# Performance work log

Measured on AMD Instinct MI355X. Metric: run time of the kernel, lower is better.

The kernel has to match this reference:

```python
import jax, jax.numpy as jnp
import numpy as np

NZ, NC = 100, 2
FEAT_NUMBER, FEATURE_DIM = 8192, 1024
B = 8192
BN_EPS = 1e-5
GUMBEL_EPS = 0.001
TEMP = 0.1


def _batchnorm(h, gamma, beta):
    # torch BatchNorm1d training mode: biased batch statistics
    mu = jnp.mean(h, axis=0, keepdims=True)
    var = jnp.var(h, axis=0, keepdims=True)
    return (h - mu) * jax.lax.rsqrt(var + BN_EPS) * gamma + beta


def setup_inputs() -> dict:
    key = jax.random.key(0)
    ks = jax.random.split(key, 16)
    def glorot(k, shape):
        lim = 1.0 / np.sqrt(shape[0])
        return jax.random.uniform(k, shape, jnp.float32, -lim, lim)
    return {
        "x": jax.random.normal(ks[0], (B, NZ), jnp.float32),
        "y": jax.random.uniform(ks[1], (B, NC), jnp.float32),
        "W1": glorot(ks[2], (NZ + NC, 256)), "b1": jnp.zeros((256,), jnp.float32),
        "g1": jnp.ones((256,), jnp.float32), "be1": jnp.zeros((256,), jnp.float32),
        "W2": glorot(ks[3], (256, 64)), "b2": jnp.zeros((64,), jnp.float32),
        "g2": jnp.ones((64,), jnp.float32), "be2": jnp.zeros((64,), jnp.float32),
        "W3": glorot(ks[4], (64, FEAT_NUMBER)), "b3": jnp.zeros((FEAT_NUMBER,), jnp.float32),
        "codebook": jax.random.normal(ks[5], (FEAT_NUMBER, FEATURE_DIM), jnp.float32),
    }


def reference(x, y, W1, b1, g1, be1, W2, b2, g2, be2, W3, b3, codebook):
    z = jnp.concatenate([x, y], axis=-1)                       # [B, nz+nc]
    h = jax.nn.relu(_batchnorm(z @ W1 + b1, g1, be1))          # [B, 256]
    h = jax.nn.relu(_batchnorm(h @ W2 + b2, g2, be2))          # [B, 64]
    logits = h @ W3 + b3                                       # [B, feat_number]

    # gumbel noise: U = eps*rand; g = -log(-log(U+eps)+eps)
    U = GUMBEL_EPS * jax.random.uniform(jax.random.key(42), logits.shape, jnp.float32)
    g = -jnp.log(-jnp.log(U + GUMBEL_EPS) + GUMBEL_EPS)
    y_soft = jax.nn.softmax((logits + g) / TEMP, axis=-1)

    # straight-through one-hot
    ind = jnp.argmax(y_soft, axis=-1)
    y_hard = jax.nn.one_hot(ind, FEAT_NUMBER, dtype=y_soft.dtype)
    z_st = jax.lax.stop_gradient(y_hard - y_soft) + y_soft     # [B, feat_number]

    # weighted codebook sum == matmul (avoids [B,F,D] broadcast intermediate)
    return jnp.einsum('bf,fd->bd', z_st, codebook)             # [B, feature_dim]
```

## Files before the change

kernel.cpp:

```cpp
#include <hip/hip_runtime.h>
#include <math.h>

#define B_ROWS   8192
#define NZ       100
#define NC       2
#define H1       256
#define H2       64
#define FEATN    8192
#define FDIM     1024
#define RROWS    16
#define NTILE    (FEATN / 16)
#define A1ROWS   16
#define A1BLKS   (B_ROWS / A1ROWS)
#define CONVBLKS 128
#define A2ROWS   16
#define A2BLKS   (B_ROWS / A2ROWS)

typedef __attribute__((ext_vector_type(8))) short short8;
typedef __attribute__((ext_vector_type(4))) float f32x4;

__device__ __forceinline__ unsigned rotl32(unsigned v, int r) {
    return (v << r) | (v >> (32 - r));
}
__device__ __forceinline__ unsigned threefry_bits(unsigned lo) {
    const unsigned ks0 = 0u, ks1 = 42u, ks2 = 0x1BD11BDAu ^ 42u;
    unsigned x0 = 0u + ks0;
    unsigned x1 = lo + ks1;
#define TF_R4(a,b,c,d) \
    x0 += x1; x1 = rotl32(x1,a); x1 ^= x0; \
    x0 += x1; x1 = rotl32(x1,b); x1 ^= x0; \
    x0 += x1; x1 = rotl32(x1,c); x1 ^= x0; \
    x0 += x1; x1 = rotl32(x1,d); x1 ^= x0;
    TF_R4(13,15,26,6);  x0 += ks1; x1 += ks2 + 1u;
    TF_R4(17,29,16,24); x0 += ks2; x1 += ks0 + 2u;
    TF_R4(13,15,26,6);  x0 += ks0; x1 += ks1 + 3u;
    TF_R4(17,29,16,24); x0 += ks1; x1 += ks2 + 4u;
    TF_R4(13,15,26,6);  x0 += ks2; x1 += ks0 + 5u;
#undef TF_R4
    return x0 ^ x1;
}
__device__ __forceinline__ float gumbel_g(unsigned flat) {
    unsigned bits = threefry_bits(flat);
    float u  = __uint_as_float((bits >> 9) | 0x3f800000u) - 1.0f;
    float U  = 0.001f * u;
    float t1 = U + 0.001f;
    float L1 = (float)log((double)t1);
    float A  = 0.001f - L1;
    float L2 = (float)log((double)A);
    return -L2;
}

__device__ __forceinline__ unsigned short f2bf(float x) {
    unsigned u = __float_as_uint(x);
    u += 0x7fffu + ((u >> 16) & 1u);
    return (unsigned short)(u >> 16);
}
__device__ __forceinline__ unsigned fmono(float x) {
    unsigned b = __float_as_uint(x);
    return (b & 0x80000000u) ? ~b : (b | 0x80000000u);
}

__global__ __launch_bounds__(512) void k_a1(
    const float* __restrict__ x, const float* __restrict__ y,
    const float* __restrict__ W1, const float* __restrict__ b1,
    const float* __restrict__ W3,
    float* __restrict__ a1, double* __restrict__ p1, double* __restrict__ p2,
    unsigned short* __restrict__ w3s, float* __restrict__ maxw)
{
    const int t = threadIdx.x;

    if (blockIdx.x >= A1BLKS) {
        const int job  = (blockIdx.x - A1BLKS) * 512 + t;
        const int T    = job >> 7;
        const int rem  = job & 127;
        const int kh   = rem >> 6;
        const int l    = rem & 63;
        const int quad = l >> 4, col = l & 15;
        const float* src = W3 + (size_t)(kh * 32 + quad * 8) * FEATN + T * 16 + col;
        unsigned short v[8];
        float mx = 0.0f;
#pragma unroll
        for (int jj = 0; jj < 8; ++jj) {
            float xv = src[(size_t)jj * FEATN];
            mx = fmaxf(mx, fabsf(xv));
            v[jj] = f2bf(xv);
        }
        uint4 o;
        o.x = (unsigned)v[0] | ((unsigned)v[1] << 16);
        o.y = (unsigned)v[2] | ((unsigned)v[3] << 16);
        o.z = (unsigned)v[4] | ((unsigned)v[5] << 16);
        o.w = (unsigned)v[6] | ((unsigned)v[7] << 16);
        ((uint4*)w3s)[job] = o;
#pragma unroll
        for (int off = 32; off; off >>= 1) mx = fmaxf(mx, __shfl_xor(mx, off));
        __shared__ float wred[8];
        if ((t & 63) == 0) wred[t >> 6] = mx;
        __syncthreads();
        if (t == 0) {
            float m = wred[0];
#pragma unroll
            for (int wq = 1; wq < 8; ++wq) m = fmaxf(m, wred[wq]);
            atomicMax((unsigned*)maxw, __float_as_uint(m));
        }
        return;
    }

    const int j    = t & 255;
    const int half = t >> 8;
    const int b0   = blockIdx.x * A1ROWS;
    const int r0   = half * 8;

    __shared__ __align__(16) float xs[NZ][16];
    __shared__ __align__(16) float ys[NC][16];
    __shared__ float vsh[256][8];
    for (int q = t; q < A1ROWS * NZ; q += 512) {
        int r = q / NZ, i = q - r * NZ;
        xs[i][r] = x[(size_t)b0 * NZ + q];
    }
    if (t < A1ROWS * NC) {
        int r = t >> 1, i = t & 1;
        ys[i][r] = y[b0 * NC + t];
    }
    __syncthreads();

    float acc[8];
#pragma unroll
    for (int r = 0; r < 8; ++r) acc[r] = 0.0f;
    for (int i = 0; i < NZ; ++i) {
        float wd = W1[i * H1 + j];
        const float4 x0 = *(const float4*)&xs[i][r0];
        const float4 x1 = *(const float4*)&xs[i][r0 + 4];
        acc[0] = fmaf(x0.x, wd, acc[0]); acc[1] = fmaf(x0.y, wd, acc[1]);
        acc[2] = fmaf(x0.z, wd, acc[2]); acc[3] = fmaf(x0.w, wd, acc[3]);
        acc[4] = fmaf(x1.x, wd, acc[4]); acc[5] = fmaf(x1.y, wd, acc[5]);
        acc[6] = fmaf(x1.z, wd, acc[6]); acc[7] = fmaf(x1.w, wd, acc[7]);
    }
#pragma unroll
    for (int i = 0; i < NC; ++i) {
        float wd = W1[(NZ + i) * H1 + j];
        const float4 y0 = *(const float4*)&ys[i][r0];
        const float4 y1 = *(const float4*)&ys[i][r0 + 4];
        acc[0] = fmaf(y0.x, wd, acc[0]); acc[1] = fmaf(y0.y, wd, acc[1]);
        acc[2] = fmaf(y0.z, wd, acc[2]); acc[3] = fmaf(y0.w, wd, acc[3]);
        acc[4] = fmaf(y1.x, wd, acc[4]); acc[5] = fmaf(y1.y, wd, acc[5]);
        acc[6] = fmaf(y1.z, wd, acc[6]); acc[7] = fmaf(y1.w, wd, acc[7]);
    }
    const float bb = b1[j];
    float v[8];
#pragma unroll
    for (int r = 0; r < 8; ++r) {
        v[r] = acc[r] + bb;
        a1[(b0 + r0 + r) * H1 + j] = v[r];
    }
    if (half) {
#pragma unroll
        for (int r = 0; r < 8; ++r) vsh[j][r] = v[r];
    }
    __syncthreads();
    if (!half) {
        double s = 0.0, s2 = 0.0;
#pragma unroll
        for (int r = 0; r < 8; ++r) {
            double dv = (double)v[r];
            s += dv; s2 += dv * dv;
        }
#pragma unroll
        for (int r = 0; r < 8; ++r) {
            double dv = (double)vsh[j][r];
            s += dv; s2 += dv * dv;
        }
        p1[blockIdx.x * H1 + j] = s;
        p2[blockIdx.x * H1 + j] = s2;
    }
}

__global__ __launch_bounds__(256) void k_stats2(
    const double* __restrict__ p1, const double* __restrict__ p2,
    int nprt, int ncol,
    const float* __restrict__ gamma, const float* __restrict__ beta,
    float* __restrict__ scale, float* __restrict__ shift)
{
    const int j = blockIdx.x, t = threadIdx.x;
    double s = 0.0, s2 = 0.0;
    for (int g = t; g < nprt; g += 256) {
        s  += p1[(size_t)g * ncol + j];
        s2 += p2[(size_t)g * ncol + j];
    }
#pragma unroll
    for (int off = 32; off; off >>= 1) {
        s  += __shfl_xor(s, off);
        s2 += __shfl_xor(s2, off);
    }
    __shared__ double ws1[4], ws2[4];
    if ((t & 63) == 0) { ws1[t >> 6] = s; ws2[t >> 6] = s2; }
    __syncthreads();
    if (t == 0) {
        s  = (ws1[0] + ws1[1]) + (ws1[2] + ws1[3]);
        s2 = (ws2[0] + ws2[1]) + (ws2[2] + ws2[3]);
        double mean = s * (1.0 / B_ROWS);
        double var  = s2 * (1.0 / B_ROWS) - mean * mean;
        double rstd = 1.0 / sqrt(var + 1e-5);
        double sc   = (double)gamma[j] * rstd;
        scale[j] = (float)sc;
        shift[j] = (float)((double)beta[j] - mean * sc);
    }
}

__global__ __launch_bounds__(512) void k_a2(
    const float* __restrict__ a1,
    const float* __restrict__ sc1, const float* __restrict__ sh1,
    const float* __restrict__ W2, const float* __restrict__ b2,
    float* __restrict__ a2, double* __restrict__ p1, double* __restrict__ p2)
{
    const int t  = threadIdx.x;
    const int k  = t & 63;
    const int rg = t >> 6;
    const int b0 = blockIdx.x * A2ROWS;
    const int r0 = rg * 2;

    __shared__ __align__(8) float hs[H1][18];
    __shared__ float vsh[64][17];

    {
        const int jc = t & 255, rq = t >> 8;
        const float sct = sc1[jc], sht = sh1[jc];
#pragma unroll
        for (int rr = rq * 8; rr < rq * 8 + 8; ++rr) {
            float vv = a1[(size_t)(b0 + rr) * H1 + jc];
            hs[jc][rr] = fmaxf(fmaf(vv, sct, sht), 0.0f);
        }
    }
    __syncthreads();

    float acc0 = 0.0f, acc1 = 0.0f;
#pragma unroll 4
    for (int j = 0; j < H1; ++j) {
        float wd = W2[j * H2 + k];
        const float2 h2 = *(const float2*)&hs[j][r0];
        acc0 = fmaf(h2.x, wd, acc0);
        acc1 = fmaf(h2.y, wd, acc1);
    }
    const float bb = b2[k];
    float v0 = acc0 + bb;
    float v1 = acc1 + bb;
    a2[(b0 + r0 + 0) * H2 + k] = v0;
    a2[(b0 + r0 + 1) * H2 + k] = v1;
    vsh[k][r0]     = v0;
    vsh[k][r0 + 1] = v1;
    __syncthreads();
    if (t < 64) {
        double s = 0.0, s2 = 0.0;
#pragma unroll
        for (int r = 0; r < A2ROWS; ++r) {
            double dv = (double)vsh[t][r];
            s += dv; s2 += dv * dv;
        }
        p1[blockIdx.x * H2 + t] = s;
        p2[blockIdx.x * H2 + t] = s2;
    }
}

__global__ __launch_bounds__(512)
__attribute__((amdgpu_waves_per_eu(4, 4)))
void k_main(
    const float* __restrict__ a2,
    const float* __restrict__ sc2, const float* __restrict__ sh2,
    const float* __restrict__ W3, const float* __restrict__ b3,
    const unsigned short* __restrict__ w3s, const float* __restrict__ maxw,
    const float* __restrict__ codebook, float* __restrict__ out)
{
    const int t    = threadIdx.x;
    const int wv   = t >> 6;
    const int lane = t & 63;
    const int quad = lane >> 4, col = lane & 15;
    const int b0   = blockIdx.x * RROWS;

    __shared__ __align__(16) float h2T[64][17];
    __shared__ float fineT[NTILE][17];
    __shared__ float thrS[RROWS];
    __shared__ unsigned long long best[RROWS];
    __shared__ unsigned short wl[RROWS * NTILE];
    __shared__ int wlN;
    __shared__ int rowInd[RROWS];
    __shared__ float maxwS;

    if (t == 0) { maxwS = maxw[0]; wlN = 0; }
    for (int q = t; q < RROWS * 64; q += 512) {
        int j = q >> 4, r = q & 15;
        float v = a2[(b0 + r) * H2 + j];
        h2T[j][r] = fmaxf(fmaf(v, sc2[j], sh2[j]), 0.0f);
    }
    __syncthreads();

    short8 aF0, aF1;
#pragma unroll
    for (int jj = 0; jj < 8; ++jj) {
        aF0[jj] = (short)f2bf(h2T[quad * 8 + jj][col]);
        aF1[jj] = (short)f2bf(h2T[32 + quad * 8 + jj][col]);
    }

    {
        const uint4*  wp = (const uint4*)w3s + (size_t)wv * 8192 + lane;
        const float4* bq = (const float4*)b3 + wv * 256 + quad;
        for (int s = 0; s < 8; ++s) {
            uint4 c[8], d[8];
            float4 bb[8];
#pragma unroll
            for (int u = 0; u < 8; ++u) {
                c[u]  = wp[u * 128];
                d[u]  = wp[u * 128 + 64];
                bb[u] = bq[u * 4];
            }
#pragma unroll
            for (int u = 0; u < 8; ++u) {
                f32x4 acc = {bb[u].x, bb[u].y, bb[u].z, bb[u].w};
                acc = __builtin_amdgcn_mfma_f32_16x16x32_bf16(
                          *(const short8*)&c[u], aF0, acc, 0, 0, 0);
                acc = __builtin_amdgcn_mfma_f32_16x16x32_bf16(
                          *(const short8*)&d[u], aF1, acc, 0, 0, 0);
                float m = fmaxf(fmaxf(acc[0], acc[1]), fmaxf(acc[2], acc[3]));
                m = fmaxf(m, __shfl_xor(m, 16));
                m = fmaxf(m, __shfl_xor(m, 32));
                if (lane < 16) fineT[(wv * 8 + s) * 8 + u][lane] = m;
            }
            wp += 1024; bq += 32;
        }
    }
    __syncthreads();

    {
        const int r = t >> 5, cc = t & 31;
        float s = fabsf(h2T[2 * cc][r]) + fabsf(h2T[2 * cc + 1][r]);
        float gmv = -1e30f;
#pragma unroll
        for (int k = 0; k < 16; ++k) gmv = fmaxf(gmv, fineT[cc + 32 * k][r]);
#pragma unroll
        for (int off = 1; off < 32; off <<= 1) {
            s   += __shfl_xor(s, off);
            gmv  = fmaxf(gmv, __shfl_xor(gmv, off));
        }
        if (cc == 0) {
            float e = s * maxwS * (1.0f / 256.0f);
            thrS[r] = gmv - (0.1068f + e + 1e-3f);
            best[r] = 0ull;
        }
    }
    __syncthreads();

    {
        const int r = t >> 5, cc = t & 31;
        const float th = thrS[r];
#pragma unroll
        for (int k = 0; k < 16; ++k) {
            const int T = cc + 32 * k;
            if (fineT[T][r] >= th) {
                int idx = atomicAdd(&wlN, 1);
                wl[idx] = (unsigned short)((r << 9) | T);
            }
        }
    }
    __syncthreads();

    {
        const int n = wlN;
        const int g = lane >> 4;
        for (int i = wv * 4; i < n; i += 32) {
            const int  ci  = i + g;
            const bool act = (ci < n);
            const int  e   = act ? wl[ci] : 0;
            const int  r   = e >> 9;
            const int  T   = e & 511;
            const int  f   = T * 16 + col;
            float acc = b3[f];
            const float* wcol = W3 + f;
#pragma unroll 8
            for (int j = 0; j < 64; ++j) {
                acc = fmaf(h2T[j][r], *wcol, acc);
                wcol += FEATN;
            }
            if (act && acc >= thrS[r]) {
                float sc = acc + gumbel_g((unsigned)(b0 + r) * (unsigned)FEATN + (unsigned)f);
                unsigned long long pk = ((unsigned long long)fmono(sc) << 32)
                                      | (unsigned)(FEATN - 1 - f);
                atomicMax(&best[r], pk);
            }
        }
    }
    __syncthreads();
    if (t < RROWS) {
        rowInd[t] = (FEATN - 1 - (int)(best[t] & 0xFFFFFFFFull)) & (FEATN - 1);
    }
    __syncthreads();

    {
        const int rr = t >> 8, tt = t & 255;
        for (int rp = 0; rp < RROWS / 2; ++rp) {
            const int r = rp * 2 + rr;
            const int ind = rowInd[r];
            const float4* src = (const float4*)(codebook + (size_t)ind * FDIM);
            float4*       dst = (float4*)(out + (size_t)(b0 + r) * FDIM);
            dst[tt] = src[tt];
        }
    }
}

extern "C" void kernel_launch(void* const* d_in, const int* in_sizes, int n_in,
                              void* d_out, int out_size, void* d_ws, size_t ws_size,
                              hipStream_t stream)
{
    const float* x   = (const float*)d_in[0];
    const float* y   = (const float*)d_in[1];
    const float* W1  = (const float*)d_in[2];
    const float* b1  = (const float*)d_in[3];
    const float* g1  = (const float*)d_in[4];
    const float* be1 = (const float*)d_in[5];
    const float* W2  = (const float*)d_in[6];
    const float* b2  = (const float*)d_in[7];
    const float* g2  = (const float*)d_in[8];
    const float* be2 = (const float*)d_in[9];
    const float* W3  = (const float*)d_in[10];
    const float* b3  = (const float*)d_in[11];
    const float* cb  = (const float*)d_in[12];
    float* out = (float*)d_out;

    float* ws  = (float*)d_ws;
    float* a1  = ws;
    float* a2  = a1 + B_ROWS * H1;
    float* sc1 = a2 + B_ROWS * H2;
    float* sh1 = sc1 + H1;
    float* sc2 = sh1 + H1;
    float* sh2 = sc2 + H2;
    double* p1 = (double*)(sh2 + H2);
    double* p2 = p1 + A1BLKS * H1;
    unsigned short* w3s = (unsigned short*)(p2 + A1BLKS * H1);
    float* maxw = (float*)(w3s + NTILE * 2 * 64 * 8);

    hipMemsetAsync(maxw, 0, 4, stream);
    k_a1    <<<A1BLKS + CONVBLKS, 512, 0, stream>>>(x, y, W1, b1, W3,
                                                    a1, p1, p2, w3s, maxw);
    k_stats2<<<H1, 256, 0, stream>>>(p1, p2, A1BLKS, H1, g1, be1, sc1, sh1);
    k_a2    <<<A2BLKS, 512, 0, stream>>>(a1, sc1, sh1, W2, b2, a2, p1, p2);
    k_stats2<<<H2, 256, 0, stream>>>(p1, p2, A2BLKS, H2, g2, be2, sc2, sh2);
    k_main  <<<B_ROWS / RROWS, 512, 0, stream>>>(a2, sc2, sh2, W3, b3,
                                                 w3s, maxw, cb, out);
}
```

Baseline: 205.1 us.

## Fuse BatchNorm statistics reduction into producer kernels via last-block tickets

```diff
diff --git a/kernel.cpp b/kernel.cpp
--- a/kernel.cpp
+++ b/kernel.cpp
@@ -60,12 +60,47 @@
     return (b & 0x80000000u) ? ~b : (b | 0x80000000u);
 }
 
+__device__ __forceinline__ void stats_tail(
+    int* cnt, int nblk, int nlast, int t,
+    const double* p1, const double* p2, int ncol,
+    const float* gamma, const float* beta,
+    float* scale, float* shift)
+{
+    __shared__ int ticket;
+    __threadfence();
+    if (t == 0) ticket = atomicAdd(cnt, 1);
+    __syncthreads();
+    const int tk = ticket;
+    if (tk < nblk - nlast) return;
+    if (t == 0) {
+        while (atomicAdd(cnt, 0) < nblk) { }
+    }
+    __syncthreads();
+    __threadfence();
+    if (t < 16) {
+        const int j = (tk - (nblk - nlast)) * 16 + t;
+        double s = 0.0, s2 = 0.0;
+        for (int g = 0; g < nblk; ++g) {
+            s  += p1[(size_t)g * ncol + j];
+            s2 += p2[(size_t)g * ncol + j];
+        }
+        double mean = s * (1.0 / B_ROWS);
+        double var  = s2 * (1.0 / B_ROWS) - mean * mean;
+        double rstd = 1.0 / sqrt(var + 1e-5);
+        double sc   = (double)gamma[j] * rstd;
+        scale[j] = (float)sc;
+        shift[j] = (float)((double)beta[j] - mean * sc);
+    }
+}
+
 __global__ __launch_bounds__(512) void k_a1(
     const float* __restrict__ x, const float* __restrict__ y,
     const float* __restrict__ W1, const float* __restrict__ b1,
     const float* __restrict__ W3,
     float* __restrict__ a1, double* __restrict__ p1, double* __restrict__ p2,
-    unsigned short* __restrict__ w3s, float* __restrict__ maxw)
+    unsigned short* __restrict__ w3s, float* __restrict__ maxw,
+    const float* __restrict__ g1, const float* __restrict__ be1,
+    float* __restrict__ sc1, float* __restrict__ sh1, int* __restrict__ cnt1)
 {
     const int t = threadIdx.x;
 
@@ -172,45 +207,17 @@
         p1[blockIdx.x * H1 + j] = s;
         p2[blockIdx.x * H1 + j] = s2;
     }
-}
-
-__global__ __launch_bounds__(256) void k_stats2(
-    const double* __restrict__ p1, const double* __restrict__ p2,
-    int nprt, int ncol,
-    const float* __restrict__ gamma, const float* __restrict__ beta,
-    float* __restrict__ scale, float* __restrict__ shift)
-{
-    const int j = blockIdx.x, t = threadIdx.x;
-    double s = 0.0, s2 = 0.0;
-    for (int g = t; g < nprt; g += 256) {
-        s  += p1[(size_t)g * ncol + j];
-        s2 += p2[(size_t)g * ncol + j];
-    }
-#pragma unroll
-    for (int off = 32; off; off >>= 1) {
-        s  += __shfl_xor(s, off);
-        s2 += __shfl_xor(s2, off);
-    }
-    __shared__ double ws1[4], ws2[4];
-    if ((t & 63) == 0) { ws1[t >> 6] = s; ws2[t >> 6] = s2; }
-    __syncthreads();
-    if (t == 0) {
-        s  = (ws1[0] + ws1[1]) + (ws1[2] + ws1[3]);
-        s2 = (ws2[0] + ws2[1]) + (ws2[2] + ws2[3]);
-        double mean = s * (1.0 / B_ROWS);
-        double var  = s2 * (1.0 / B_ROWS) - mean * mean;
-        double rstd = 1.0 / sqrt(var + 1e-5);
-        double sc   = (double)gamma[j] * rstd;
-        scale[j] = (float)sc;
-        shift[j] = (float)((double)beta[j] - mean * sc);
-    }
+
+    stats_tail(cnt1, A1BLKS, 16, t, p1, p2, H1, g1, be1, sc1, sh1);
 }
 
 __global__ __launch_bounds__(512) void k_a2(
     const float* __restrict__ a1,
     const float* __restrict__ sc1, const float* __restrict__ sh1,
     const float* __restrict__ W2, const float* __restrict__ b2,
-    float* __restrict__ a2, double* __restrict__ p1, double* __restrict__ p2)
+    float* __restrict__ a2, double* __restrict__ p1, double* __restrict__ p2,
+    const float* __restrict__ g2, const float* __restrict__ be2,
+    float* __restrict__ sc2, float* __restrict__ sh2, int* __restrict__ cnt2)
 {
     const int t  = threadIdx.x;
     const int k  = t & 63;
@@ -258,6 +265,8 @@
         p1[blockIdx.x * H2 + t] = s;
         p2[blockIdx.x * H2 + t] = s2;
     }
+
+    stats_tail(cnt2, A2BLKS, 4, t, p1, p2, H2, g2, be2, sc2, sh2);
 }
 
 __global__ __launch_bounds__(512)
@@ -434,13 +443,15 @@
     double* p2 = p1 + A1BLKS * H1;
     unsigned short* w3s = (unsigned short*)(p2 + A1BLKS * H1);
     float* maxw = (float*)(w3s + NTILE * 2 * 64 * 8);
-
-    hipMemsetAsync(maxw, 0, 4, stream);
-    k_a1    <<<A1BLKS + CONVBLKS, 512, 0, stream>>>(x, y, W1, b1, W3,
-                                                    a1, p1, p2, w3s, maxw);
-    k_stats2<<<H1, 256, 0, stream>>>(p1, p2, A1BLKS, H1, g1, be1, sc1, sh1);
-    k_a2    <<<A2BLKS, 512, 0, stream>>>(a1, sc1, sh1, W2, b2, a2, p1, p2);
-    k_stats2<<<H2, 256, 0, stream>>>(p1, p2, A2BLKS, H2, g2, be2, sc2, sh2);
-    k_main  <<<B_ROWS / RROWS, 512, 0, stream>>>(a2, sc2, sh2, W3, b3,
-                                                 w3s, maxw, cb, out);
-}
+    int*   cnt1 = (int*)(maxw + 1);
+    int*   cnt2 = cnt1 + 1;
+
+    hipMemsetAsync(maxw, 0, 12, stream);
+    k_a1 <<<A1BLKS + CONVBLKS, 512, 0, stream>>>(x, y, W1, b1, W3,
+                                                 a1, p1, p2, w3s, maxw,
+                                                 g1, be1, sc1, sh1, cnt1);
+    k_a2 <<<A2BLKS, 512, 0, stream>>>(a1, sc1, sh1, W2, b2, a2, p1, p2,
+                                      g2, be2, sc2, sh2, cnt2);
+    k_main <<<B_ROWS / RROWS, 512, 0, stream>>>(a2, sc2, sh2, W3, b3,
+                                                w3s, maxw, cb, out);
+}
```

After: 416.3 us. 103% more time.
